# Performance work log

Measured on AMD Instinct MI355X. Metric: run time of the kernel, lower is better.

Reference implementation:

```python
import jax, jax.numpy as jnp
import numpy as np

NUM_HEADS = 16
WINDOW = 32
HIDDEN = 1024
HEAD_DIM = HIDDEN // NUM_HEADS


def setup_inputs() -> dict:
    key = jax.random.key(0)
    ks = jax.random.split(key, 9)
    B, S, H = 2, 2048, HIDDEN
    s = 0.02
    return {
        "hidden_states": jax.random.normal(ks[0], (B, S, H), jnp.float32),
        "Wq": jax.random.normal(ks[1], (H, H), jnp.float32) * s,
        "bq": jnp.zeros((H,), jnp.float32),
        "Wk": jax.random.normal(ks[2], (H, H), jnp.float32) * s,
        "bk": jnp.zeros((H,), jnp.float32),
        "Wv": jax.random.normal(ks[3], (H, H), jnp.float32) * s,
        "bv": jnp.zeros((H,), jnp.float32),
        "Wo": jax.random.normal(ks[4], (H, H), jnp.float32) * s,
        "bo": jnp.zeros((H,), jnp.float32),
    }


def reference(hidden_states, Wq, bq, Wk, bk, Wv, bv, Wo, bo):
    B, S, H = hidden_states.shape
    scale = jnp.sqrt(jnp.asarray(HEAD_DIM, hidden_states.dtype))
    # torch Linear: x @ W.T + b
    q = (hidden_states @ Wq.T + bq).reshape(B, S, NUM_HEADS, HEAD_DIM)
    k = (hidden_states @ Wk.T + bk).reshape(B, S, NUM_HEADS, HEAD_DIM)
    v = (hidden_states @ Wv.T + bv).reshape(B, S, NUM_HEADS, HEAD_DIM)
    # Full scores; block-causal pattern: query in block bi sees keys in blocks <= bi.
    scores = jnp.einsum("bihd,bjhd->bhij", q, k) / scale  # [B,H,S,S]
    blk = jnp.arange(S) // WINDOW
    allowed = blk[:, None] >= blk[None, :]  # [S,S]
    # Faithful to original: unfilled (future-block) entries are ZERO, not -inf,
    # and still participate in the softmax.
    scores = jnp.where(allowed, scores, jnp.zeros((), scores.dtype))
    probs = jax.nn.softmax(scores, axis=-1)
    ctx = jnp.einsum("bhij,bjhd->bihd", probs, v).reshape(B, S, H)
    return ctx @ Wo.T + bo
```

## Files before the change

### kernel.cpp

```cpp
#include <hip/hip_runtime.h>
#include <cstdint>

namespace {

constexpr int kS   = 2048;
constexpr int kNH  = 16;
constexpr int kHD  = 64;
constexpr int kH   = 1024;
constexpr int kB   = 2;
constexpr int kWin = 32;
constexpr int kNBlk = kS / kWin;
constexpr float kQScale = 0.18033688011112042f;

typedef __attribute__((ext_vector_type(8))) short short8v;
typedef __attribute__((ext_vector_type(4))) float f32x4;
typedef __attribute__((ext_vector_type(4))) unsigned short u16x4;
typedef __attribute__((ext_vector_type(8))) unsigned short u16x8;
typedef __attribute__((ext_vector_type(2))) unsigned int u32x2;

static __device__ __forceinline__ unsigned short f2bf(float f) {
  unsigned int u = __float_as_uint(f);
  return (unsigned short)((u + 0x7fffu + ((u >> 16) & 1u)) >> 16);
}
static __device__ __forceinline__ float bf2f(unsigned short b) {
  return __uint_as_float((unsigned int)b << 16);
}
static __device__ __forceinline__ void async16(const void* g, void* l) {
  __builtin_amdgcn_global_load_lds((__attribute__((address_space(1))) void*)(g),
                                   (__attribute__((address_space(3))) void*)(l),
                                   16, 0, 0);
}

__global__ __launch_bounds__(256) void cvt_bf16(
    const float* __restrict__ hs, const float* __restrict__ Wq,
    const float* __restrict__ Wk, const float* __restrict__ Wv,
    const float* __restrict__ Wo, unsigned short* __restrict__ out)
{
  const size_t idx = ((size_t)blockIdx.x * 256 + threadIdx.x) * 8;
  const int seg = (int)(idx >> 20);
  const size_t off = idx & ((1u << 20) - 1);
  const float* src;
  if (seg < 4)       src = hs + idx;
  else if (seg == 4) src = Wq + off;
  else if (seg == 5) src = Wk + off;
  else if (seg == 6) src = Wv + off;
  else               src = Wo + off;
  const float4 f0 = *(const float4*)(src);
  const float4 f1 = *(const float4*)(src + 4);
  u16x8 pk;
  pk[0] = f2bf(f0.x); pk[1] = f2bf(f0.y); pk[2] = f2bf(f0.z); pk[3] = f2bf(f0.w);
  pk[4] = f2bf(f1.x); pk[5] = f2bf(f1.y); pk[6] = f2bf(f1.z); pk[7] = f2bf(f1.w);
  *(u16x8*)(out + idx) = pk;
}

template <int MT, int EPI>
__global__ __launch_bounds__(256) void gemm_mfma(
    const unsigned short* __restrict__ A, const unsigned short* __restrict__ W,
    const float* __restrict__ b0, const float* __restrict__ b1,
    const float* __restrict__ b2, float* __restrict__ Cf,
    unsigned short* __restrict__ Dq, unsigned short* __restrict__ Dk,
    unsigned short* __restrict__ Dv, int M, int N, int K)
{
  constexpr int BMr = MT * 32;
  __shared__ unsigned short As[BMr * 64];
  __shared__ unsigned short Ws[128 * 64];
  const int tid  = threadIdx.x;
  const int wave = tid >> 6, lane = tid & 63;
  const int q16  = lane & 15, quad = lane >> 4;
  const int wm   = wave & 1,  wn   = wave >> 1;
  const int bm = blockIdx.y * BMr, bn = blockIdx.x * 128;

  const int lrow8 = lane >> 3;
  const int lch   = lane & 7;
  const int gch   = lch ^ lrow8;

  const unsigned short* gA[MT];
  unsigned short* lA[MT];
#pragma unroll
  for (int g = 0; g < MT; ++g) {
    const int row0 = wave * MT * 8 + g * 8;
    gA[g] = A + (size_t)(bm + row0 + lrow8) * K + gch * 8;
    lA[g] = As + row0 * 64;
  }
  const unsigned short* gW[4];
  unsigned short* lW[4];
#pragma unroll
  for (int g = 0; g < 4; ++g) {
    const int row0 = wave * 32 + g * 8;
    gW[g] = W + (size_t)(bn + row0 + lrow8) * K + gch * 8;
    lW[g] = Ws + row0 * 64;
  }

  const unsigned short* fA = As + (wm * (MT * 16) + q16) * 64;
  const unsigned short* fB = Ws + (wn * 64 + q16) * 64;
  const int sl0 = ((quad)     ^ (q16 & 7)) * 8;
  const int sl1 = ((quad + 4) ^ (q16 & 7)) * 8;

  const f32x4 zero = {0.f, 0.f, 0.f, 0.f};
  f32x4 acc[MT][4];
#pragma unroll
  for (int i = 0; i < MT; ++i)
#pragma unroll
    for (int j = 0; j < 4; ++j) acc[i][j] = zero;

  for (int k0 = 0; k0 < K; k0 += 64) {
    __syncthreads();
#pragma unroll
    for (int g = 0; g < MT; ++g) { async16(gA[g], lA[g]); gA[g] += 64; }
#pragma unroll
    for (int g = 0; g < 4; ++g)  { async16(gW[g], lW[g]); gW[g] += 64; }
    __syncthreads();

    short8v a[MT], b[4];
#pragma unroll
    for (int t = 0; t < MT; ++t) a[t] = *(const short8v*)(fA + t * 16 * 64 + sl0);
#pragma unroll
    for (int t = 0; t < 4; ++t)  b[t] = *(const short8v*)(fB + t * 16 * 64 + sl0);
#pragma unroll
    for (int mt = 0; mt < MT; ++mt)
#pragma unroll
      for (int nt = 0; nt < 4; ++nt)
        acc[mt][nt] = __builtin_amdgcn_mfma_f32_16x16x32_bf16(a[mt], b[nt], acc[mt][nt], 0, 0, 0);
#pragma unroll
    for (int t = 0; t < MT; ++t) a[t] = *(const short8v*)(fA + t * 16 * 64 + sl1);
#pragma unroll
    for (int t = 0; t < 4; ++t)  b[t] = *(const short8v*)(fB + t * 16 * 64 + sl1);
#pragma unroll
    for (int mt = 0; mt < MT; ++mt)
#pragma unroll
      for (int nt = 0; nt < 4; ++nt)
        acc[mt][nt] = __builtin_amdgcn_mfma_f32_16x16x32_bf16(a[mt], b[nt], acc[mt][nt], 0, 0, 0);
  }

#pragma unroll
  for (int nt = 0; nt < 4; ++nt) {
    const int col = bn + wn * 64 + nt * 16 + q16;
#pragma unroll
    for (int mt = 0; mt < MT; ++mt) {
      const int row0 = bm + wm * (MT * 16) + mt * 16 + quad * 4;
      const f32x4 av = acc[mt][nt];
      if (EPI == 0) {
        const float bv = b0[col];
#pragma unroll
        for (int r = 0; r < 4; ++r)
          Cf[(size_t)(row0 + r) * N + col] = av[r] + bv;
      } else {
        const int mat = col >> 10, c = col & 1023;
        const int b = row0 >> 11, s0 = row0 & 2047;
        const int h = c >> 6, d = c & 63;
        const size_t bhslot = (size_t)(b * kNH + h);
        if (mat == 0) {
          const float bv = b0[c];
          unsigned short* base = Dq + ((bhslot * kS + s0) * kHD + d);
#pragma unroll
          for (int r = 0; r < 4; ++r) base[(size_t)r * kHD] = f2bf((av[r] + bv) * kQScale);
        } else if (mat == 1) {
          const float bv = b1[c];
          unsigned short* base = Dk + ((bhslot * kS + s0) * kHD + d);
#pragma unroll
          for (int r = 0; r < 4; ++r) base[(size_t)r * kHD] = f2bf(av[r] + bv);
        } else {
          const float bv = b2[c];
          u16x4 pk;
          pk[0] = f2bf(av[0] + bv); pk[1] = f2bf(av[1] + bv);
          pk[2] = f2bf(av[2] + bv); pk[3] = f2bf(av[3] + bv);
          *(u16x4*)(Dv + (bhslot * kHD + d) * kS + s0) = pk;
        }
      }
    }
  }
}

__global__ __launch_bounds__(256) void vprefix_kernel(
    const unsigned short* __restrict__ vt, float* __restrict__ vrest)
{
  __shared__ float bsum[64][64];
  __shared__ float ptot[4][64];
  const int bh = blockIdx.x;
  const int d = threadIdx.x & 63, part = threadIdx.x >> 6;
  const unsigned short* base = vt + ((size_t)bh * kHD + d) * kS;
#pragma unroll 4
  for (int j = 0; j < 16; ++j) {
    const int jb = part * 16 + j;
    const unsigned short* p = base + jb * kWin;
    float s = 0.f;
#pragma unroll
    for (int i = 0; i < 4; ++i) {
      const u16x8 v = *(const u16x8*)(p + i * 8);
#pragma unroll
      for (int e = 0; e < 8; ++e) s += bf2f(v[e]);
    }
    bsum[jb][d] = s;
  }
  __syncthreads();
  float t = 0.f;
#pragma unroll
  for (int j = 0; j < 16; ++j) t += bsum[part * 16 + j][d];
  ptot[part][d] = t;
  __syncthreads();
  float s = 0.f;
  for (int p2 = part + 1; p2 < 4; ++p2) s += ptot[p2][d];
#pragma unroll
  for (int j = 15; j >= 0; --j) {
    const int bi = part * 16 + j;
    vrest[((size_t)bh * kNBlk + bi) * kHD + d] = s;
    s += bsum[bi][d];
  }
}

template <int QT0>
__device__ __forceinline__ void attn_iter(
    const unsigned short* __restrict__ Kb, const unsigned short* __restrict__ Vtb,
    int jb, const short8v qf[4][2], unsigned short* __restrict__ esw,
    int q16, int quad, int swz, f32x4 acc[4][4], float dAcc[4])
{
  const unsigned short* Kj = Kb + (size_t)jb * kWin * kHD;
  short8v kf[2][2];
#pragma unroll
  for (int kt = 0; kt < 2; ++kt)
#pragma unroll
    for (int ks = 0; ks < 2; ++ks)
      kf[kt][ks] = *(const short8v*)(Kj + (kt * 16 + q16) * kHD + ks * 32 + quad * 8);

  const f32x4 zero = {0.f, 0.f, 0.f, 0.f};
#pragma unroll
  for (int kt = 0; kt < 2; ++kt) {
    f32x4 st[4];
#pragma unroll
    for (int qt = QT0; qt < 4; ++qt) {
      f32x4 c = zero;
      c = __builtin_amdgcn_mfma_f32_16x16x32_bf16(kf[kt][0], qf[qt][0], c, 0, 0, 0);
      c = __builtin_amdgcn_mfma_f32_16x16x32_bf16(kf[kt][1], qf[qt][1], c, 0, 0, 0);
      st[qt] = c;
    }
    const int g = kt * 2 + (quad >> 1);
    const int col = ((g ^ swz) * 8) + (quad & 1) * 4;
#pragma unroll
    for (int qt = QT0; qt < 4; ++qt) {
      const float e0 = __builtin_amdgcn_exp2f(st[qt][0]);
      const float e1 = __builtin_amdgcn_exp2f(st[qt][1]);
      const float e2 = __builtin_amdgcn_exp2f(st[qt][2]);
      const float e3 = __builtin_amdgcn_exp2f(st[qt][3]);
      dAcc[qt] += (e0 + e1) + (e2 + e3);
      const unsigned int r0 = __float_as_uint(e0) + 0x8000u;
      const unsigned int r1 = __float_as_uint(e1) + 0x8000u;
      const unsigned int r2 = __float_as_uint(e2) + 0x8000u;
      const unsigned int r3 = __float_as_uint(e3) + 0x8000u;
      u32x2 w;
      w[0] = __builtin_amdgcn_perm(r1, r0, 0x07060302u);
      w[1] = __builtin_amdgcn_perm(r3, r2, 0x07060302u);
      *(u32x2*)(esw + (qt * 16 + q16) * 32 + col) = w;
    }
  }
  short8v vf[4];
#pragma unroll
  for (int nt = 0; nt < 4; ++nt)
    vf[nt] = *(const short8v*)(Vtb + (size_t)(nt * 16 + q16) * kS +
                               jb * kWin + quad * 8);
  short8v af[4];
#pragma unroll
  for (int mt = QT0; mt < 4; ++mt)
    af[mt] = *(const short8v*)(esw + (mt * 16 + q16) * 32 + (quad ^ swz) * 8);
#pragma unroll
  for (int nt = 0; nt < 4; ++nt) {
#pragma unroll
    for (int mt = QT0; mt < 4; ++mt)
      acc[mt][nt] = __builtin_amdgcn_mfma_f32_16x16x32_bf16(af[mt], vf[nt], acc[mt][nt], 0, 0, 0);
  }
}

__global__ __launch_bounds__(256, 3) void attn_mfma(
    const unsigned short* __restrict__ qb, const unsigned short* __restrict__ kb,
    const unsigned short* __restrict__ vtb, const float* __restrict__ vrest,
    unsigned short* __restrict__ ctx)
{
  __shared__ union SM {
    unsigned short es[4][2048];
    float part[4096];
  } sm;
  __shared__ float den[4][64];

  const int tid  = threadIdx.x;
  const int wave = tid >> 6;
  const int lane = tid & 63;
  const int q16  = lane & 15;
  const int quad = lane >> 4;
  const int bh = blockIdx.x & 31;
  const int pr = 31 - (blockIdx.x >> 5);
  const int bilo = pr * 2, bihi = pr * 2 + 1;
  const int b  = bh >> 4, h = bh & 15;

  const unsigned short* Qb  = qb  + ((size_t)bh * kS + (size_t)pr * 64) * kHD;
  const unsigned short* Kb  = kb  + (size_t)bh * kS * kHD;
  const unsigned short* Vtb = vtb + (size_t)bh * kHD * kS;

  short8v qf[4][2];
#pragma unroll
  for (int qt = 0; qt < 4; ++qt)
#pragma unroll
    for (int ks = 0; ks < 2; ++ks)
      qf[qt][ks] = *(const short8v*)(Qb + (qt * 16 + q16) * kHD + ks * 32 + quad * 8);

  const f32x4 zero = {0.f, 0.f, 0.f, 0.f};
  f32x4 acc[4][4];
#pragma unroll
  for (int mt = 0; mt < 4; ++mt)
#pragma unroll
    for (int nt = 0; nt < 4; ++nt) acc[mt][nt] = zero;
  float dAcc[4] = {0.f, 0.f, 0.f, 0.f};

  unsigned short* esw = sm.es[wave];
  const int swz = (q16 >> 2) & 3;

  for (int jb = wave; jb <= bilo; jb += 4)
    attn_iter<0>(Kb, Vtb, jb, qf, esw, q16, quad, swz, acc, dAcc);
  if ((bihi & 3) == wave)
    attn_iter<2>(Kb, Vtb, bihi, qf, esw, q16, quad, swz, acc, dAcc);

#pragma unroll
  for (int qt = 0; qt < 4; ++qt) {
    dAcc[qt] += __shfl_xor(dAcc[qt], 16);
    dAcc[qt] += __shfl_xor(dAcc[qt], 32);
  }

  __syncthreads();
  if (quad == 0) {
#pragma unroll
    for (int qt = 0; qt < 4; ++qt) den[wave][qt * 16 + q16] = dAcc[qt];
  }
  if (wave == 0) {
#pragma unroll
    for (int mt = 0; mt < 4; ++mt)
#pragma unroll
      for (int nt = 0; nt < 4; ++nt)
#pragma unroll
        for (int r = 0; r < 4; ++r)
          sm.part[((mt * 4 + nt) * 4 + r) * 64 + lane] = acc[mt][nt][r];
  }
  __syncthreads();
  if (wave == 1) {
#pragma unroll
    for (int mt = 0; mt < 4; ++mt)
#pragma unroll
      for (int nt = 0; nt < 4; ++nt)
#pragma unroll
        for (int r = 0; r < 4; ++r)
          sm.part[((mt * 4 + nt) * 4 + r) * 64 + lane] += acc[mt][nt][r];
  }
  __syncthreads();
  if (wave == 2) {
#pragma unroll
    for (int mt = 0; mt < 4; ++mt)
#pragma unroll
      for (int nt = 0; nt < 4; ++nt)
#pragma unroll
        for (int r = 0; r < 4; ++r)
          sm.part[((mt * 4 + nt) * 4 + r) * 64 + lane] += acc[mt][nt][r];
  }
  __syncthreads();
  if (wave == 3) {
#pragma unroll
    for (int mt = 0; mt < 4; ++mt)
#pragma unroll
      for (int nt = 0; nt < 4; ++nt)
#pragma unroll
        for (int r = 0; r < 4; ++r)
          sm.part[((mt * 4 + nt) * 4 + r) * 64 + lane] += acc[mt][nt][r];
  }
  __syncthreads();

  {
    const int nt = wave;
    const int dim = nt * 16 + q16;
    const float vrlo = vrest[((size_t)bh * kNBlk + bilo) * kHD + dim];
    const float vrhi = vrest[((size_t)bh * kNBlk + bihi) * kHD + dim];
    const float nrlo = 32.0f * (float)((kNBlk - 1) - bilo);
    const float nrhi = 32.0f * (float)((kNBlk - 1) - bihi);
    unsigned short* outb = ctx + ((size_t)b * kS + (size_t)pr * 64) * kH + h * kHD;
#pragma unroll
    for (int mt = 0; mt < 4; ++mt) {
      const float vr = (mt < 2) ? vrlo : vrhi;
      const float nr = (mt < 2) ? nrlo : nrhi;
#pragma unroll
      for (int r = 0; r < 4; ++r) {
        const int idx = ((mt * 4 + nt) * 4 + r) * 64 + lane;
        const int qrow = mt * 16 + quad * 4 + r;
        const float dsum = den[0][qrow] + den[1][qrow] +
                           den[2][qrow] + den[3][qrow] + nr;
        outb[(size_t)qrow * kH + dim] = f2bf((sm.part[idx] + vr) / dsum);
      }
    }
  }
}

}

extern "C" void kernel_launch(void* const* d_in, const int* in_sizes, int n_in,
                              void* d_out, int out_size, void* d_ws, size_t ws_size,
                              hipStream_t stream) {
  const float* hs = (const float*)d_in[0];
  const float* Wq = (const float*)d_in[1];
  const float* bq = (const float*)d_in[2];
  const float* Wk = (const float*)d_in[3];
  const float* bk = (const float*)d_in[4];
  const float* Wv = (const float*)d_in[5];
  const float* bv = (const float*)d_in[6];
  const float* Wo = (const float*)d_in[7];
  const float* bo = (const float*)d_in[8];

  char* wsb = (char*)d_ws;
  unsigned short* hsb   = (unsigned short*)(wsb);
  unsigned short* wqkv  = hsb + (4u << 20);
  unsigned short* wob   = hsb + (7u << 20);
  unsigned short* qbuf  = (unsigned short*)(wsb + (16u << 20));
  unsigned short* kbuf  = (unsigned short*)(wsb + (24u << 20));
  unsigned short* vtbuf = (unsigned short*)(wsb + (32u << 20));
  unsigned short* ctxb  = (unsigned short*)(wsb + (40u << 20));
  float*          vrest = (float*)         (wsb + (48u << 20));

  const int M = kB * kS;

  cvt_bf16<<<4096, 256, 0, stream>>>(hs, Wq, Wk, Wv, Wo, hsb);
  gemm_mfma<4, 1><<<dim3(3072 / 128, M / 128), 256, 0, stream>>>(
      hsb, wqkv, bq, bk, bv, nullptr, qbuf, kbuf, vtbuf, M, 3072, kH);
  vprefix_kernel<<<kB * kNH, 256, 0, stream>>>(vtbuf, vrest);
  attn_mfma<<<(kNBlk / 2) * kB * kNH, 256, 0, stream>>>(qbuf, kbuf, vtbuf, vrest, ctxb);
  gemm_mfma<2, 0><<<dim3(kH / 128, M / 64), 256, 0, stream>>>(
      ctxb, wob, bo, nullptr, nullptr, (float*)d_out, nullptr, nullptr, nullptr,
      M, kH, kH);
}
```

Measured before the change: 194.7 us.

## Double-buffer GEMM LDS tiles with async prefetch of next K-slice

Restructures the bf16 MFMA GEMM main loop to use two LDS buffers with 32-wide K slices instead of one 64-wide buffer. The next slice is prefetched asynchronously while the current one is consumed, which removes one of the two barriers per iteration and overlaps global-to-LDS loads with MFMA work. The LDS layout and XOR swizzle are changed to fit the 32-element rows. The cost is twice as many loop iterations with less MFMA work each, and correctness now depends on the async loads completing before the barrier.

```diff
diff --git a/kernel.cpp b/kernel.cpp
--- a/kernel.cpp
+++ b/kernel.cpp
@@ -62,39 +62,34 @@
     unsigned short* __restrict__ Dv, int M, int N, int K)
 {
   constexpr int BMr = MT * 32;
-  __shared__ unsigned short As[BMr * 64];
-  __shared__ unsigned short Ws[128 * 64];
+  constexpr int AG  = MT / 2;
+  __shared__ unsigned short As[2][BMr * 32];
+  __shared__ unsigned short Ws[2][128 * 32];
   const int tid  = threadIdx.x;
   const int wave = tid >> 6, lane = tid & 63;
   const int q16  = lane & 15, quad = lane >> 4;
   const int wm   = wave & 1,  wn   = wave >> 1;
   const int bm = blockIdx.y * BMr, bn = blockIdx.x * 128;
 
-  const int lrow8 = lane >> 3;
-  const int lch   = lane & 7;
-  const int gch   = lch ^ lrow8;
-
-  const unsigned short* gA[MT];
-  unsigned short* lA[MT];
-#pragma unroll
-  for (int g = 0; g < MT; ++g) {
-    const int row0 = wave * MT * 8 + g * 8;
-    gA[g] = A + (size_t)(bm + row0 + lrow8) * K + gch * 8;
-    lA[g] = As + row0 * 64;
-  }
-  const unsigned short* gW[4];
-  unsigned short* lW[4];
-#pragma unroll
-  for (int g = 0; g < 4; ++g) {
-    const int row0 = wave * 32 + g * 8;
-    gW[g] = W + (size_t)(bn + row0 + lrow8) * K + gch * 8;
-    lW[g] = Ws + row0 * 64;
-  }
-
-  const unsigned short* fA = As + (wm * (MT * 16) + q16) * 64;
-  const unsigned short* fB = Ws + (wn * 64 + q16) * 64;
-  const int sl0 = ((quad)     ^ (q16 & 7)) * 8;
-  const int sl1 = ((quad + 4) ^ (q16 & 7)) * 8;
+  const int lrow   = lane >> 2;
+  const int lchunk = (lane & 3) ^ ((lane >> 3) & 3);
+
+  const unsigned short* gA[AG];
+  int lAoff[AG];
+#pragma unroll
+  for (int g = 0; g < AG; ++g) {
+    const int row0 = wave * 16 * AG + g * 16;
+    gA[g] = A + (size_t)(bm + row0 + lrow) * K + lchunk * 8;
+    lAoff[g] = row0 * 32;
+  }
+  const unsigned short* gW0 = W + (size_t)(bn + wave * 32 + lrow) * K + lchunk * 8;
+  const unsigned short* gW1 = gW0 + (size_t)16 * K;
+  const int lW0off = (wave * 32) * 32;
+  const int lW1off = lW0off + 16 * 32;
+
+  const int swz = quad ^ ((q16 >> 1) & 3);
+  const int fAoff = (wm * (MT * 16) + q16) * 32 + swz * 8;
+  const int fBoff = (wn * 64 + q16) * 32 + swz * 8;
 
   const f32x4 zero = {0.f, 0.f, 0.f, 0.f};
   f32x4 acc[MT][4];
@@ -103,33 +98,33 @@
 #pragma unroll
     for (int j = 0; j < 4; ++j) acc[i][j] = zero;
 
-  for (int k0 = 0; k0 < K; k0 += 64) {
+#pragma unroll
+  for (int g = 0; g < AG; ++g) { async16(gA[g], &As[0][lAoff[g]]); gA[g] += 32; }
+  async16(gW0, &Ws[0][lW0off]); gW0 += 32;
+  async16(gW1, &Ws[0][lW1off]); gW1 += 32;
+
+  int buf = 0;
+  for (int k0 = 0; k0 < K; k0 += 32) {
     __syncthreads();
-#pragma unroll
-    for (int g = 0; g < MT; ++g) { async16(gA[g], lA[g]); gA[g] += 64; }
-#pragma unroll
-    for (int g = 0; g < 4; ++g)  { async16(gW[g], lW[g]); gW[g] += 64; }
-    __syncthreads();
-
+    if (k0 + 32 < K) {
+#pragma unroll
+      for (int g = 0; g < AG; ++g) { async16(gA[g], &As[buf ^ 1][lAoff[g]]); gA[g] += 32; }
+      async16(gW0, &Ws[buf ^ 1][lW0off]); gW0 += 32;
+      async16(gW1, &Ws[buf ^ 1][lW1off]); gW1 += 32;
+    }
+    const unsigned short* fA = &As[buf][fAoff];
+    const unsigned short* fB = &Ws[buf][fBoff];
     short8v a[MT], b[4];
 #pragma unroll
-    for (int t = 0; t < MT; ++t) a[t] = *(const short8v*)(fA + t * 16 * 64 + sl0);
-#pragma unroll
-    for (int t = 0; t < 4; ++t)  b[t] = *(const short8v*)(fB + t * 16 * 64 + sl0);
+    for (int t = 0; t < MT; ++t) a[t] = *(const short8v*)(fA + t * 16 * 32);
+#pragma unroll
+    for (int t = 0; t < 4; ++t)  b[t] = *(const short8v*)(fB + t * 16 * 32);
 #pragma unroll
     for (int mt = 0; mt < MT; ++mt)
 #pragma unroll
       for (int nt = 0; nt < 4; ++nt)
         acc[mt][nt] = __builtin_amdgcn_mfma_f32_16x16x32_bf16(a[mt], b[nt], acc[mt][nt], 0, 0, 0);
-#pragma unroll
-    for (int t = 0; t < MT; ++t) a[t] = *(const short8v*)(fA + t * 16 * 64 + sl1);
-#pragma unroll
-    for (int t = 0; t < 4; ++t)  b[t] = *(const short8v*)(fB + t * 16 * 64 + sl1);
-#pragma unroll
-    for (int mt = 0; mt < MT; ++mt)
-#pragma unroll
-      for (int nt = 0; nt < 4; ++nt)
-        acc[mt][nt] = __builtin_amdgcn_mfma_f32_16x16x32_bf16(a[mt], b[nt], acc[mt][nt], 0, 0, 0);
+    buf ^= 1;
   }
 
 #pragma unroll
```

New measurement: 198.8 us. +2.1%, slower.

## Double-buffer QKV GEMM LDS tiles and process attention in 64-key chunks

Applied to the files above, without the earlier changes.

The QKV projection GEMM now uses two LDS buffers with K-steps of 32, prefetching the next tile while MFMAs run on the current one and using one barrier per step instead of two. The output projection keeps the old single-buffered kernel as a separate, simplified specialization. The attention inner loop now handles 64 keys per iteration instead of 32, with a larger per-wave LDS scratch, which halves the loop trip count and amortizes V/K loads. The cost is more LDS use, which can lower occupancy, and more, smaller K-steps in the QKV GEMM.

```diff
diff --git a/kernel.cpp b/kernel.cpp
--- a/kernel.cpp
+++ b/kernel.cpp
@@ -54,7 +54,7 @@
 }
 
 template <int MT, int EPI>
-__global__ __launch_bounds__(256) void gemm_mfma(
+__global__ __launch_bounds__(256) void gemm_dbuf(
     const unsigned short* __restrict__ A, const unsigned short* __restrict__ W,
     const float* __restrict__ b0, const float* __restrict__ b1,
     const float* __restrict__ b2, float* __restrict__ Cf,
@@ -62,39 +62,34 @@
     unsigned short* __restrict__ Dv, int M, int N, int K)
 {
   constexpr int BMr = MT * 32;
-  __shared__ unsigned short As[BMr * 64];
-  __shared__ unsigned short Ws[128 * 64];
+  constexpr int AG  = MT / 2;
+  __shared__ unsigned short As[2][BMr * 32];
+  __shared__ unsigned short Ws[2][128 * 32];
   const int tid  = threadIdx.x;
   const int wave = tid >> 6, lane = tid & 63;
   const int q16  = lane & 15, quad = lane >> 4;
   const int wm   = wave & 1,  wn   = wave >> 1;
   const int bm = blockIdx.y * BMr, bn = blockIdx.x * 128;
 
-  const int lrow8 = lane >> 3;
-  const int lch   = lane & 7;
-  const int gch   = lch ^ lrow8;
-
-  const unsigned short* gA[MT];
-  unsigned short* lA[MT];
-#pragma unroll
-  for (int g = 0; g < MT; ++g) {
-    const int row0 = wave * MT * 8 + g * 8;
-    gA[g] = A + (size_t)(bm + row0 + lrow8) * K + gch * 8;
-    lA[g] = As + row0 * 64;
-  }
-  const unsigned short* gW[4];
-  unsigned short* lW[4];
-#pragma unroll
-  for (int g = 0; g < 4; ++g) {
-    const int row0 = wave * 32 + g * 8;
-    gW[g] = W + (size_t)(bn + row0 + lrow8) * K + gch * 8;
-    lW[g] = Ws + row0 * 64;
-  }
-
-  const unsigned short* fA = As + (wm * (MT * 16) + q16) * 64;
-  const unsigned short* fB = Ws + (wn * 64 + q16) * 64;
-  const int sl0 = ((quad)     ^ (q16 & 7)) * 8;
-  const int sl1 = ((quad + 4) ^ (q16 & 7)) * 8;
+  const int lrow   = lane >> 2;
+  const int lchunk = (lane & 3) ^ ((lane >> 3) & 3);
+
+  const unsigned short* gA[AG];
+  int lAoff[AG];
+#pragma unroll
+  for (int g = 0; g < AG; ++g) {
+    const int row0 = wave * 16 * AG + g * 16;
+    gA[g] = A + (size_t)(bm + row0 + lrow) * K + lchunk * 8;
+    lAoff[g] = row0 * 32;
+  }
+  const unsigned short* gW0 = W + (size_t)(bn + wave * 32 + lrow) * K + lchunk * 8;
+  const unsigned short* gW1 = gW0 + (size_t)16 * K;
+  const int lW0off = (wave * 32) * 32;
+  const int lW1off = lW0off + 16 * 32;
+
+  const int swz = quad ^ ((q16 >> 1) & 3);
+  const int fAoff = (wm * (MT * 16) + q16) * 32 + swz * 8;
+  const int fBoff = (wn * 64 + q16) * 32 + swz * 8;
 
   const f32x4 zero = {0.f, 0.f, 0.f, 0.f};
   f32x4 acc[MT][4];
@@ -103,33 +98,33 @@
 #pragma unroll
     for (int j = 0; j < 4; ++j) acc[i][j] = zero;
 
-  for (int k0 = 0; k0 < K; k0 += 64) {
+#pragma unroll
+  for (int g = 0; g < AG; ++g) { async16(gA[g], &As[0][lAoff[g]]); gA[g] += 32; }
+  async16(gW0, &Ws[0][lW0off]); gW0 += 32;
+  async16(gW1, &Ws[0][lW1off]); gW1 += 32;
+
+  int buf = 0;
+  for (int k0 = 0; k0 < K; k0 += 32) {
     __syncthreads();
-#pragma unroll
-    for (int g = 0; g < MT; ++g) { async16(gA[g], lA[g]); gA[g] += 64; }
-#pragma unroll
-    for (int g = 0; g < 4; ++g)  { async16(gW[g], lW[g]); gW[g] += 64; }
-    __syncthreads();
-
+    if (k0 + 32 < K) {
+#pragma unroll
+      for (int g = 0; g < AG; ++g) { async16(gA[g], &As[buf ^ 1][lAoff[g]]); gA[g] += 32; }
+      async16(gW0, &Ws[buf ^ 1][lW0off]); gW0 += 32;
+      async16(gW1, &Ws[buf ^ 1][lW1off]); gW1 += 32;
+    }
+    const unsigned short* fA = &As[buf][fAoff];
+    const unsigned short* fB = &Ws[buf][fBoff];
     short8v a[MT], b[4];
 #pragma unroll
-    for (int t = 0; t < MT; ++t) a[t] = *(const short8v*)(fA + t * 16 * 64 + sl0);
-#pragma unroll
-    for (int t = 0; t < 4; ++t)  b[t] = *(const short8v*)(fB + t * 16 * 64 + sl0);
+    for (int t = 0; t < MT; ++t) a[t] = *(const short8v*)(fA + t * 16 * 32);
+#pragma unroll
+    for (int t = 0; t < 4; ++t)  b[t] = *(const short8v*)(fB + t * 16 * 32);
 #pragma unroll
     for (int mt = 0; mt < MT; ++mt)
 #pragma unroll
       for (int nt = 0; nt < 4; ++nt)
         acc[mt][nt] = __builtin_amdgcn_mfma_f32_16x16x32_bf16(a[mt], b[nt], acc[mt][nt], 0, 0, 0);
-#pragma unroll
-    for (int t = 0; t < MT; ++t) a[t] = *(const short8v*)(fA + t * 16 * 64 + sl1);
-#pragma unroll
-    for (int t = 0; t < 4; ++t)  b[t] = *(const short8v*)(fB + t * 16 * 64 + sl1);
-#pragma unroll
-    for (int mt = 0; mt < MT; ++mt)
-#pragma unroll
-      for (int nt = 0; nt < 4; ++nt)
-        acc[mt][nt] = __builtin_amdgcn_mfma_f32_16x16x32_bf16(a[mt], b[nt], acc[mt][nt], 0, 0, 0);
+    buf ^= 1;
   }
 
 #pragma unroll
@@ -167,6 +162,97 @@
           *(u16x4*)(Dv + (bhslot * kHD + d) * kS + s0) = pk;
         }
       }
+    }
+  }
+}
+
+template <int MT, int EPI>
+__global__ __launch_bounds__(256) void gemm_std(
+    const unsigned short* __restrict__ A, const unsigned short* __restrict__ W,
+    const float* __restrict__ b0, float* __restrict__ Cf, int M, int N, int K)
+{
+  constexpr int BMr = MT * 32;
+  __shared__ unsigned short As[BMr * 64];
+  __shared__ unsigned short Ws[128 * 64];
+  const int tid  = threadIdx.x;
+  const int wave = tid >> 6, lane = tid & 63;
+  const int q16  = lane & 15, quad = lane >> 4;
+  const int wm   = wave & 1,  wn   = wave >> 1;
+  const int bm = blockIdx.y * BMr, bn = blockIdx.x * 128;
+
+  const int lrow8 = lane >> 3;
+  const int lch   = lane & 7;
+  const int gch   = lch ^ lrow8;
+
+  const unsigned short* gA[MT];
+  unsigned short* lA[MT];
+#pragma unroll
+  for (int g = 0; g < MT; ++g) {
+    const int row0 = wave * MT * 8 + g * 8;
+    gA[g] = A + (size_t)(bm + row0 + lrow8) * K + gch * 8;
+    lA[g] = As + row0 * 64;
+  }
+  const unsigned short* gW[4];
+  unsigned short* lW[4];
+#pragma unroll
+  for (int g = 0; g < 4; ++g) {
+    const int row0 = wave * 32 + g * 8;
+    gW[g] = W + (size_t)(bn + row0 + lrow8) * K + gch * 8;
+    lW[g] = Ws + row0 * 64;
+  }
+
+  const unsigned short* fA = As + (wm * (MT * 16) + q16) * 64;
+  const unsigned short* fB = Ws + (wn * 64 + q16) * 64;
+  const int sl0 = ((quad)     ^ (q16 & 7)) * 8;
+  const int sl1 = ((quad + 4) ^ (q16 & 7)) * 8;
+
+  const f32x4 zero = {0.f, 0.f, 0.f, 0.f};
+  f32x4 acc[MT][4];
+#pragma unroll
+  for (int i = 0; i < MT; ++i)
+#pragma unroll
+    for (int j = 0; j < 4; ++j) acc[i][j] = zero;
+
+  for (int k0 = 0; k0 < K; k0 += 64) {
+    __syncthreads();
+#pragma unroll
+    for (int g = 0; g < MT; ++g) { async16(gA[g], lA[g]); gA[g] += 64; }
+#pragma unroll
+    for (int g = 0; g < 4; ++g)  { async16(gW[g], lW[g]); gW[g] += 64; }
+    __syncthreads();
+
+    short8v a[MT], b[4];
+#pragma unroll
+    for (int t = 0; t < MT; ++t) a[t] = *(const short8v*)(fA + t * 16 * 64 + sl0);
+#pragma unroll
+    for (int t = 0; t < 4; ++t)  b[t] = *(const short8v*)(fB + t * 16 * 64 + sl0);
+#pragma unroll
+    for (int mt = 0; mt < MT; ++mt)
+#pragma unroll
+      for (int nt = 0; nt < 4; ++nt)
+        acc[mt][nt] = __builtin_amdgcn_mfma_f32_16x16x32_bf16(a[mt], b[nt], acc[mt][nt], 0, 0, 0);
+#pragma unroll
+    for (int t = 0; t < MT; ++t) a[t] = *(const short8v*)(fA + t * 16 * 64 + sl1);
+#pragma unroll
+    for (int t = 0; t < 4; ++t)  b[t] = *(const short8v*)(fB + t * 16 * 64 + sl1);
+#pragma unroll
+    for (int mt = 0; mt < MT; ++mt)
+#pragma unroll
+      for (int nt = 0; nt < 4; ++nt)
+        acc[mt][nt] = __builtin_amdgcn_mfma_f32_16x16x32_bf16(a[mt], b[nt], acc[mt][nt], 0, 0, 0);
+  }
+
+#pragma unroll
+  for (int nt = 0; nt < 4; ++nt) {
+    const int col = bn + wn * 64 + nt * 16 + q16;
+    const float bv = b0[col];
+#pragma unroll
+    for (int mt = 0; mt < MT; ++mt) {
+      const int row0 = bm + wm * (MT * 16) + mt * 16 + quad * 4;
+      const f32x4 av = acc[mt][nt];
+#pragma unroll
+      for (int r = 0; r < 4; ++r)
+        Cf[(size_t)(row0 + r) * N + col] = av[r] + bv;
     }
   }
 }
@@ -208,64 +294,74 @@
   }
 }
 
-template <int QT0>
-__device__ __forceinline__ void attn_iter(
+template <int FULL>
+__device__ __forceinline__ void attn_iter64(
     const unsigned short* __restrict__ Kb, const unsigned short* __restrict__ Vtb,
-    int jb, const short8v qf[4][2], unsigned short* __restrict__ esw,
+    int J, const short8v qf[4][2], unsigned short* __restrict__ esw,
     int q16, int quad, int swz, f32x4 acc[4][4], float dAcc[4])
 {
-  const unsigned short* Kj = Kb + (size_t)jb * kWin * kHD;
-  short8v kf[2][2];
-#pragma unroll
-  for (int kt = 0; kt < 2; ++kt)
-#pragma unroll
-    for (int ks = 0; ks < 2; ++ks)
-      kf[kt][ks] = *(const short8v*)(Kj + (kt * 16 + q16) * kHD + ks * 32 + quad * 8);
-
   const f32x4 zero = {0.f, 0.f, 0.f, 0.f};
-#pragma unroll
-  for (int kt = 0; kt < 2; ++kt) {
-    f32x4 st[4];
-#pragma unroll
-    for (int qt = QT0; qt < 4; ++qt) {
-      f32x4 c = zero;
-      c = __builtin_amdgcn_mfma_f32_16x16x32_bf16(kf[kt][0], qf[qt][0], c, 0, 0, 0);
-      c = __builtin_amdgcn_mfma_f32_16x16x32_bf16(kf[kt][1], qf[qt][1], c, 0, 0, 0);
-      st[qt] = c;
+  const unsigned short* Kj = Kb + (size_t)J * 64 * kHD;
+
+#pragma unroll
+  for (int half = 0; half < 2; ++half) {
+    const int qt0 = (FULL || half == 0) ? 0 : 2;
+    short8v kf[2][2];
+#pragma unroll
+    for (int t = 0; t < 2; ++t)
+#pragma unroll
+      for (int ks = 0; ks < 2; ++ks)
+        kf[t][ks] = *(const short8v*)(Kj + ((half * 2 + t) * 16 + q16) * kHD +
+                                      ks * 32 + quad * 8);
+#pragma unroll
+    for (int t = 0; t < 2; ++t) {
+      f32x4 st[4];
+#pragma unroll
+      for (int qt = qt0; qt < 4; ++qt) {
+        f32x4 c = zero;
+        c = __builtin_amdgcn_mfma_f32_16x16x32_bf16(kf[t][0], qf[qt][0], c, 0, 0, 0);
+        c = __builtin_amdgcn_mfma_f32_16x16x32_bf16(kf[t][1], qf[qt][1], c, 0, 0, 0);
+        st[qt] = c;
+      }
+      const int kc = (half * 2 + t) * 2 + (quad >> 1);
+      const int col = ((kc ^ swz) * 8) + (quad & 1) * 4;
+#pragma unroll
+      for (int qt = qt0; qt < 4; ++qt) {
+        const float e0 = __builtin_amdgcn_exp2f(st[qt][0]);
+        const float e1 = __builtin_amdgcn_exp2f(st[qt][1]);
+        const float e2 = __builtin_amdgcn_exp2f(st[qt][2]);
+        const float e3 = __builtin_amdgcn_exp2f(st[qt][3]);
+        dAcc[qt] += (e0 + e1) + (e2 + e3);
+        const unsigned int r0 = __float_as_uint(e0) + 0x8000u;
+        const unsigned int r1 = __float_as_uint(e1) + 0x8000u;
+        const unsigned int r2 = __float_as_uint(e2) + 0x8000u;
+        const unsigned int r3 = __float_as_uint(e3) + 0x8000u;
+        u32x2 w;
+        w[0] = __builtin_amdgcn_perm(r1, r0, 0x07060302u);
+        w[1] = __builtin_amdgcn_perm(r3, r2, 0x07060302u);
+        *(u32x2*)(esw + (qt * 16 + q16) * 64 + col) = w;
+      }
     }
-    const int g = kt * 2 + (quad >> 1);
-    const int col = ((g ^ swz) * 8) + (quad & 1) * 4;
-#pragma unroll
-    for (int qt = QT0; qt < 4; ++qt) {
-      const float e0 = __builtin_amdgcn_exp2f(st[qt][0]);
-      const float e1 = __builtin_amdgcn_exp2f(st[qt][1]);
-      const float e2 = __builtin_amdgcn_exp2f(st[qt][2]);
-      const float e3 = __builtin_amdgcn_exp2f(st[qt][3]);
-      dAcc[qt] += (e0 + e1) + (e2 + e3);
-      const unsigned int r0 = __float_as_uint(e0) + 0x8000u;
-      const unsigned int r1 = __float_as_uint(e1) + 0x8000u;
-      const unsigned int r2 = __float_as_uint(e2) + 0x8000u;
-      const unsigned int r3 = __float_as_uint(e3) + 0x8000u;
-      u32x2 w;
-      w[0] = __builtin_amdgcn_perm(r1, r0, 0x07060302u);
-      w[1] = __builtin_amdgcn_perm(r3, r2, 0x07060302u);
-      *(u32x2*)(esw + (qt * 16 + q16) * 32 + col) = w;
-    }
-  }
-  short8v vf[4];
-#pragma unroll
-  for (int nt = 0; nt < 4; ++nt)
-    vf[nt] = *(const short8v*)(Vtb + (size_t)(nt * 16 + q16) * kS +
-                               jb * kWin + quad * 8);
-  short8v af[4];
-#pragma unroll
-  for (int mt = QT0; mt < 4; ++mt)
-    af[mt] = *(const short8v*)(esw + (mt * 16 + q16) * 32 + (quad ^ swz) * 8);
-#pragma unroll
-  for (int nt = 0; nt < 4; ++nt) {
-#pragma unroll
-    for (int mt = QT0; mt < 4; ++mt)
-      acc[mt][nt] = __builtin_amdgcn_mfma_f32_16x16x32_bf16(af[mt], vf[nt], acc[mt][nt], 0, 0, 0);
+  }
+
+#pragma unroll
+  for (int c = 0; c < 2; ++c) {
+    const int mt0 = (FULL || c == 0) ? 0 : 2;
+    short8v vf[4];
+#pragma unroll
+    for (int nt = 0; nt < 4; ++nt)
+      vf[nt] = *(const short8v*)(Vtb + (size_t)(nt * 16 + q16) * kS +
+                                 J * 64 + c * 32 + quad * 8);
+    short8v af[4];
+#pragma unroll
+    for (int mt = mt0; mt < 4; ++mt)
+      af[mt] = *(const short8v*)(esw + (mt * 16 + q16) * 64 +
+                                 (((c * 4 + quad) ^ swz) * 8));
+#pragma unroll
+    for (int nt = 0; nt < 4; ++nt)
+#pragma unroll
+      for (int mt = mt0; mt < 4; ++mt)
+        acc[mt][nt] = __builtin_amdgcn_mfma_f32_16x16x32_bf16(af[mt], vf[nt], acc[mt][nt], 0, 0, 0);
   }
 }
 
@@ -275,7 +371,7 @@
     unsigned short* __restrict__ ctx)
 {
   __shared__ union SM {
-    unsigned short es[4][2048];
+    unsigned short es[4][4096];
     float part[4096];
   } sm;
   __shared__ float den[4][64];
@@ -310,12 +406,12 @@
   float dAcc[4] = {0.f, 0.f, 0.f, 0.f};
 
   unsigned short* esw = sm.es[wave];
-  const int swz = (q16 >> 2) & 3;
-
-  for (int jb = wave; jb <= bilo; jb += 4)
-    attn_iter<0>(Kb, Vtb, jb, qf, esw, q16, quad, swz, acc, dAcc);
-  if ((bihi & 3) == wave)
-    attn_iter<2>(Kb, Vtb, bihi, qf, esw, q16, quad, swz, acc, dAcc);
+  const int swz = q16 & 7;
+
+  for (int J = wave; J < pr; J += 4)
+    attn_iter64<1>(Kb, Vtb, J, qf, esw, q16, quad, swz, acc, dAcc);
+  if ((pr & 3) == wave)
+    attn_iter64<0>(Kb, Vtb, pr, qf, esw, q16, quad, swz, acc, dAcc);
 
 #pragma unroll
   for (int qt = 0; qt < 4; ++qt) {
@@ -421,11 +517,10 @@
   const int M = kB * kS;
 
   cvt_bf16<<<4096, 256, 0, stream>>>(hs, Wq, Wk, Wv, Wo, hsb);
-  gemm_mfma<4, 1><<<dim3(3072 / 128, M / 128), 256, 0, stream>>>(
+  gemm_dbuf<4, 1><<<dim3(3072 / 128, M / 128), 256, 0, stream>>>(
       hsb, wqkv, bq, bk, bv, nullptr, qbuf, kbuf, vtbuf, M, 3072, kH);
   vprefix_kernel<<<kB * kNH, 256, 0, stream>>>(vtbuf, vrest);
   attn_mfma<<<(kNBlk / 2) * kB * kNH, 256, 0, stream>>>(qbuf, kbuf, vtbuf, vrest, ctxb);
-  gemm_mfma<2, 0><<<dim3(kH / 128, M / 64), 256, 0, stream>>>(
-      ctxb, wob, bo, nullptr, nullptr, (float*)d_out, nullptr, nullptr, nullptr,
-      M, kH, kH);
-}
+  gemm_std<2, 0><<<dim3(kH / 128, M / 64), 256, 0, stream>>>(
+      ctxb, wob, bo, (float*)d_out, M, kH, kH);
+}
```

After: 214.8 us. +10.3%, slower.
